# Kernel optimization log

Measured on AMD Instinct MI355X. Metric: run time of the kernel, lower is better.

Reference implementation:

```python
import jax, jax.numpy as jnp
import numpy as np

THRESH = 1e-6
EPS = 1e-8
LN_EPS = 1e-5


def _layer(h, M, W_in, b_in, W_out, b_out, W_self, b_self, gamma, beta):
    # Normalize incoming flows per destination column: A[j,i] = M[j,i]/sum_k M[k,i]
    A = M / (jnp.sum(M, axis=0, keepdims=True) + EPS)
    mask = A > THRESH
    W = jnp.where(mask, A, 0.0)                      # thresholded edge weights [N,N]
    T = h @ W_in + b_in                              # transformed features [N,out]
    weighted_sum = jnp.einsum('ji,jd->id', W, T)     # sum over origins j per dest i
    weight_sum = jnp.sum(W, axis=0)                  # [N]
    has_edge = jnp.any(mask, axis=0)                 # dest i has >=1 incoming edge
    agg = jnp.where(has_edge[:, None],
                    weighted_sum / (weight_sum[:, None] + EPS),
                    T)
    agg = agg @ W_out + b_out                        # dropout is identity in eval
    out = agg + (h @ W_self + b_self)                # residual (dims differ -> self_transform)
    mu = jnp.mean(out, axis=-1, keepdims=True)
    var = jnp.mean(jnp.square(out - mu), axis=-1, keepdims=True)
    out = (out - mu) * jax.lax.rsqrt(var + LN_EPS) * gamma + beta
    return out


def setup_inputs() -> dict:
    key = jax.random.key(0)
    ks = jax.random.split(key, 16)
    N, D_IN, D_H, D_OUT = 8192, 256, 512, 256
    s = 0.05
    return {
        'node_features': jax.random.normal(ks[0], (N, D_IN), jnp.float32),
        'mobility_matrix': jax.random.uniform(ks[1], (N, N), jnp.float32),
        # layer 1: in -> hidden
        'W_in1': jax.random.normal(ks[2], (D_IN, D_H)) * s,
        'b_in1': jnp.zeros((D_H,)),
        'W_out1': jax.random.normal(ks[3], (D_H, D_H)) * s,
        'b_out1': jnp.zeros((D_H,)),
        'W_self1': jax.random.normal(ks[4], (D_IN, D_H)) * s,
        'b_self1': jnp.zeros((D_H,)),
        'g1': jnp.ones((D_H,)),
        'be1': jnp.zeros((D_H,)),
        # layer 2: hidden -> out
        'W_in2': jax.random.normal(ks[5], (D_H, D_OUT)) * s,
        'b_in2': jnp.zeros((D_OUT,)),
        'W_out2': jax.random.normal(ks[6], (D_OUT, D_OUT)) * s,
        'b_out2': jnp.zeros((D_OUT,)),
        'W_self2': jax.random.normal(ks[7], (D_H, D_OUT)) * s,
        'b_self2': jnp.zeros((D_OUT,)),
        'g2': jnp.ones((D_OUT,)),
        'be2': jnp.zeros((D_OUT,)),
    }


def reference(node_features, mobility_matrix,
              W_in1, b_in1, W_out1, b_out1, W_self1, b_self1, g1, be1,
              W_in2, b_in2, W_out2, b_out2, W_self2, b_self2, g2, be2):
    h = _layer(node_features, mobility_matrix,
               W_in1, b_in1, W_out1, b_out1, W_self1, b_self1, g1, be1)
    h = jax.nn.relu(h)  # inter-layer activation
    h = _layer(h, mobility_matrix,
               W_in2, b_in2, W_out2, b_out2, W_self2, b_self2, g2, be2)
    h = jax.nn.relu(h)  # final activation
    return h
```

## Files before the change

### kernel.cpp

```cpp
#include <hip/hip_runtime.h>
#include <stdint.h>

typedef short bf16x8 __attribute__((ext_vector_type(8)));
typedef short s16x4 __attribute__((ext_vector_type(4)));
typedef float f32x4 __attribute__((ext_vector_type(4)));
typedef unsigned int u32;
typedef unsigned char u8;

#define EPS_A 1e-8f
#define THR_A 1e-6f
#define NN 8192

static __device__ __forceinline__ short f2bf(float f) {
  u32 u = __float_as_uint(f);
  u = u + 0x7FFFu + ((u >> 16) & 1u);
  return (short)(u >> 16);
}
static __device__ __forceinline__ float bf2f(short s) {
  return __uint_as_float(((u32)(unsigned short)s) << 16);
}
static __device__ __forceinline__ u8 f2fp8(float v) {
  return (u8)(__builtin_amdgcn_cvt_pk_fp8_f32(v, v, 0, false) & 0xff);
}
static __device__ __forceinline__ void gld16(const void* g, void* l) {
  __builtin_amdgcn_global_load_lds(
      (const __attribute__((address_space(1))) u32*)g,
      (__attribute__((address_space(3))) u32*)l, 16, 0, 0);
}

__global__ __launch_bounds__(256) void k_prep_all(
    const float* __restrict__ Mob, const float* __restrict__ nf,
    const float* __restrict__ W_in1, const float* __restrict__ W_out1,
    const float* __restrict__ W_self1, const float* __restrict__ W_in2,
    const float* __restrict__ W_out2, const float* __restrict__ W_self2,
    const float* __restrict__ b_in1, const float* __restrict__ b_out1,
    const float* __restrict__ b_self1, const float* __restrict__ b_out2,
    const float* __restrict__ b_self2,
    u8* __restrict__ Mt8, float* __restrict__ colsum, u32* __restrict__ colmax,
    u8* __restrict__ nft8, short* __restrict__ A1cat, short* __restrict__ Win1b,
    short* __restrict__ Wout1t, short* __restrict__ Bcat1, short* __restrict__ Win2t,
    short* __restrict__ Bcat2, float* __restrict__ bias1c, float* __restrict__ bias2c)
{
  __shared__ __align__(16) u32 sbuf[256 * 17];
  int b = blockIdx.x;
  const int t = threadIdx.x;
  if (b < 4096) {
    const int i0 = (b & 31) * 256;
    const int j0 = (b >> 5) * 64;
    const int i = i0 + t;
    float s = 0.f, mx = 0.f;
    #pragma unroll 4
    for (int j4 = 0; j4 < 16; ++j4) {
      float v0 = Mob[(size_t)(j0 + j4 * 4 + 0) * NN + i];
      float v1 = Mob[(size_t)(j0 + j4 * 4 + 1) * NN + i];
      float v2 = Mob[(size_t)(j0 + j4 * 4 + 2) * NN + i];
      float v3 = Mob[(size_t)(j0 + j4 * 4 + 3) * NN + i];
      s += v0 + v1 + v2 + v3;
      mx = fmaxf(fmaxf(mx, fmaxf(v0, v1)), fmaxf(v2, v3));
      u32 pk = __builtin_amdgcn_cvt_pk_fp8_f32(v0, v1, 0, false);
      pk = __builtin_amdgcn_cvt_pk_fp8_f32(v2, v3, (int)pk, true);
      sbuf[t * 17 + j4] = pk;
    }
    atomicAdd(&colsum[i], s);
    atomicMax(&colmax[i], __float_as_uint(mx));
    __syncthreads();
    #pragma unroll
    for (int p = 0; p < 4; ++p) {
      const int r = p * 64 + (t >> 2);
      const int c = t & 3;
      const u32* src = &sbuf[r * 17 + c * 4];
      int4 w = make_int4(src[0], src[1], src[2], src[3]);
      *(int4*)&Mt8[(size_t)(i0 + r) * NN + j0 + c * 16] = w;
    }
    return;
  }
  b -= 4096;
  if (b < 512) {
    u8* tile = (u8*)sbuf;
    const int r0 = (b & 127) * 64, c0 = (b >> 7) * 64;
    #pragma unroll
    for (int p = 0; p < 16; ++p) {
      const int rr = p * 4 + (t >> 6), cc = t & 63;
      tile[rr * 68 + cc] = f2fp8(nf[(size_t)(r0 + rr) * 256 + c0 + cc]);
    }
    __syncthreads();
    #pragma unroll
    for (int q = 0; q < 16; ++q) {
      const int cc = q * 4 + (t >> 6), rr = t & 63;
      nft8[(size_t)(c0 + cc) * 8192 + r0 + rr] = tile[rr * 68 + cc];
    }
    return;
  }
  b -= 512;
  if (b < 2048) {
    const int idx = b * 256 + t;
    const float4 v = ((const float4*)nf)[idx];
    const int i = idx >> 6;
    const int c = (idx & 63) * 4;
    s16x4 o;
    o.x = f2bf(v.x); o.y = f2bf(v.y); o.z = f2bf(v.z); o.w = f2bf(v.w);
    *(s16x4*)&A1cat[(size_t)i * 512 + 256 + c] = o;
    return;
  }
  b -= 2048;
  if (b < 128) {
    const int idx = b * 256 + t;
    const float4 v = ((const float4*)W_in1)[idx];
    s16x4 o;
    o.x = f2bf(v.x); o.y = f2bf(v.y); o.z = f2bf(v.z); o.w = f2bf(v.w);
    *(s16x4*)&Win1b[idx * 4] = o;
    return;
  }
  b -= 128;
  if (b < 1024) {
    const int idx = b * 256 + t;
    const int r = idx >> 9, c = idx & 511;
    Wout1t[(size_t)c * 512 + r] = f2bf(W_out1[idx]);
    return;
  }
  b -= 1024;
  if (b < 512) {
    const int idx = b * 256 + t;
    const int r = idx >> 9, c = idx & 511;
    Bcat1[(size_t)c * 512 + 256 + r] = f2bf(W_self1[idx]);
    return;
  }
  b -= 512;
  if (b < 512) {
    const int idx = b * 256 + t;
    const int r = idx >> 8, c = idx & 255;
    Win2t[(size_t)c * 512 + r] = f2bf(W_in2[idx]);
    return;
  }
  b -= 512;
  if (b < 256) {
    const int idx = b * 256 + t;
    const int r = idx >> 8, c = idx & 255;
    Bcat2[(size_t)c * 768 + r] = f2bf(W_out2[idx]);
    return;
  }
  b -= 256;
  if (b < 512) {
    const int idx = b * 256 + t;
    const int r = idx >> 8, c = idx & 255;
    Bcat2[(size_t)c * 768 + 256 + r] = f2bf(W_self2[idx]);
    return;
  }
  b -= 512;
  if (b < 2) {
    const int n = b * 256 + t;
    float a = b_out1[n] + b_self1[n];
    for (int p = 0; p < 512; ++p) a += b_in1[p] * W_out1[(size_t)p * 512 + n];
    bias1c[n] = a;
    return;
  }
  bias2c[t] = b_out2[t] + b_self2[t];
}

__global__ __launch_bounds__(256) void k_gemm_raw_n(
    const short* __restrict__ A, const short* __restrict__ B, int K, int ldA, int ldB,
    short* __restrict__ C, int ldC)
{
  constexpr int LDP = 40;
  __shared__ __align__(16) short As[64 * LDP];
  __shared__ __align__(16) short Bs[64 * LDP];
  const int t = threadIdx.x;
  const int m0 = blockIdx.y * 64, n0 = blockIdx.x * 64;
  const int wid = t >> 6, l = t & 63;
  const int wr = wid >> 1, wc = wid & 1;
  const int lr = l & 15, lk = l >> 4;
  f32x4 acc[2][2] = {};
  const int sr = t >> 2;
  const int sc = (t & 3) * 8;
  const short* gA0 = A + (size_t)(m0 + sr) * ldA + sc;
  const short* gB0 = B + (size_t)(n0 + sr) * ldB + sc;
  for (int k0 = 0; k0 < K; k0 += 32) {
    const int4 a0 = *(const int4*)(gA0 + k0);
    const int4 b0 = *(const int4*)(gB0 + k0);
    __syncthreads();
    *(int4*)&As[sr * LDP + sc] = a0;
    *(int4*)&Bs[sr * LDP + sc] = b0;
    __syncthreads();
    bf16x8 av[2], bv[2];
    #pragma unroll
    for (int mi = 0; mi < 2; ++mi)
      av[mi] = *(const bf16x8*)&As[(wr * 32 + mi * 16 + lr) * LDP + lk * 8];
    #pragma unroll
    for (int ni = 0; ni < 2; ++ni)
      bv[ni] = *(const bf16x8*)&Bs[(wc * 32 + ni * 16 + lr) * LDP + lk * 8];
    #pragma unroll
    for (int mi = 0; mi < 2; ++mi)
      #pragma unroll
      for (int ni = 0; ni < 2; ++ni)
        acc[mi][ni] = __builtin_amdgcn_mfma_f32_16x16x32_bf16(av[mi], bv[ni], acc[mi][ni], 0, 0, 0);
  }
  #pragma unroll
  for (int mi = 0; mi < 2; ++mi)
    #pragma unroll
    for (int r = 0; r < 4; ++r) {
      const int m = m0 + wr * 32 + mi * 16 + lk * 4 + r;
      #pragma unroll
      for (int ni = 0; ni < 2; ++ni) {
        const int n = n0 + wc * 32 + ni * 16 + lr;
        C[(size_t)m * ldC + n] = f2bf(acc[mi][ni][r]);
      }
    }
}

template <int BN, int EPI>
__global__ __launch_bounds__(256) void k_g64(
    const short* __restrict__ A, const short* __restrict__ B, int K, int ldA, int ldB,
    void* __restrict__ Cout, int ldC, const float* __restrict__ bias0,
    u8* __restrict__ C8)
{
  constexpr int ROWS = 64 + BN;
  constexpr int CH = ROWS / 32;
  constexpr int NI = BN / 32;
  __shared__ __align__(16) short S[ROWS * 64];
  const int t = threadIdx.x;

  const int gx = gridDim.x;
  int flat = blockIdx.y * gx + blockIdx.x;
  const int cpx = (gx * gridDim.y) >> 3;
  flat = (flat & 7) * cpx + (flat >> 3);
  const int bx = flat % gx, by = flat / gx;
  const int m0 = by * 64, n0 = bx * BN;

  const int wid = t >> 6, l = t & 63;
  const int wr = wid >> 1, wc = wid & 1;
  const int lr = l & 15, lk = l >> 4;

  f32x4 acc[2][NI] = {};

  const int lrow = l >> 3, lcol = l & 7;
  const int wbase = wid * (ROWS / 4);
  short* dbase = S + wbase * 64;
  const short* gsrc[CH];
  #pragma unroll
  for (int c = 0; c < CH; ++c) {
    const int ar = wbase + c * 8 + lrow;
    const int scol = (lcol ^ (ar & 7)) * 8;
    gsrc[c] = (ar < 64) ? A + (size_t)(m0 + ar) * ldA + scol
                        : B + (size_t)(n0 + ar - 64) * ldB + scol;
  }

  const int niters = K >> 6;
  int kk = flat % niters;
  for (int it = 0; it < niters; ++it) {
    const int koff = kk << 6;
    kk = (kk + 1 == niters) ? 0 : kk + 1;
    __syncthreads();
    #pragma unroll
    for (int c = 0; c < CH; ++c)
      gld16(gsrc[c] + koff, dbase + c * 512);
    __syncthreads();

    __builtin_amdgcn_s_setprio(1);
    #pragma unroll
    for (int ks = 0; ks < 2; ++ks) {
      bf16x8 av[2], bv[NI];
      #pragma unroll
      for (int mi = 0; mi < 2; ++mi) {
        const int row = wr * 32 + mi * 16 + lr;
        av[mi] = *(const bf16x8*)&S[row * 64 + ((ks * 4 + lk) ^ (row & 7)) * 8];
      }
      #pragma unroll
      for (int ni = 0; ni < NI; ++ni) {
        const int row = 64 + wc * (BN / 2) + ni * 16 + lr;
        bv[ni] = *(const bf16x8*)&S[row * 64 + ((ks * 4 + lk) ^ (row & 7)) * 8];
      }
      #pragma unroll
      for (int mi = 0; mi < 2; ++mi)
        #pragma unroll
        for (int ni = 0; ni < NI; ++ni)
          acc[mi][ni] = __builtin_amdgcn_mfma_f32_16x16x32_bf16(av[mi], bv[ni], acc[mi][ni], 0, 0, 0);
    }
    __builtin_amdgcn_s_setprio(0);
  }

  #pragma unroll
  for (int mi = 0; mi < 2; ++mi) {
    #pragma unroll
    for (int r = 0; r < 4; ++r) {
      const int m = m0 + wr * 32 + mi * 16 + lk * 4 + r;
      float bm = 0.f;
      if (EPI == 0 || EPI == 4) bm = bias0[m];
      #pragma unroll
      for (int ni = 0; ni < NI; ++ni) {
        const int n = n0 + wc * (BN / 2) + ni * 16 + lr;
        float v = acc[mi][ni][r];
        if (EPI == 0 || EPI == 4) {
          v += bm;
          ((short*)Cout)[(size_t)m * ldC + n] = f2bf(v);
          if (EPI == 4) C8[(size_t)m * ldC + n] = f2fp8(v);
        } else {
          ((float*)Cout)[(size_t)m * ldC + n] = v + bias0[n];
        }
      }
    }
  }
}

__global__ __launch_bounds__(256) void k_sk128_f8(
    const u8* __restrict__ A, const u8* __restrict__ B, int K, int ldA, int ldB,
    short* __restrict__ P, int ldC, size_t pstride)
{
  __shared__ __align__(16) u8 As[128 * 64];
  __shared__ __align__(16) u8 Bs[128 * 64];
  const int t = threadIdx.x;

  const int sk = blockIdx.z;
  A += (size_t)sk * K;
  B += (size_t)sk * K;

  const int gx = gridDim.x;
  int flat = blockIdx.y * gx + blockIdx.x;
  const int cpx = (gx * gridDim.y) >> 3;
  flat = (flat & 7) * cpx + (flat >> 3);
  const int bx = flat % gx, by = flat / gx;
  const int m0 = by * 128, n0 = bx * 128;

  const int wid = t >> 6, l = t & 63;
  const int wr = wid >> 1, wc = wid & 1;
  const int lr = l & 15, lk = l >> 4;

  f32x4 acc[4][4] = {};

  const int side = wid >> 1;
  const int hrow = (wid & 1) * 64;
  const u8* Xp = side ? B : A;
  const int ldX = side ? ldB : ldA;
  const int x0 = side ? n0 : m0;
  u8* dbase = (side ? Bs : As) + hrow * 64;
  const u8* gsrc[4];
  #pragma unroll
  for (int c = 0; c < 4; ++c) {
    const int row = hrow + c * 16 + (l >> 2);
    const int ql = (l & 3) ^ (row & 3);
    gsrc[c] = Xp + (size_t)(x0 + row) * ldX + ql * 16;
  }

  const int niters = K >> 6;
  int kk = (flat + sk * 3) & (niters - 1);
  for (int it = 0; it < niters; ++it) {
    const int koff = kk << 6;
    kk = (kk + 1) & (niters - 1);
    __syncthreads();
    gld16(gsrc[0] + koff, dbase);
    gld16(gsrc[1] + koff, dbase + 1024);
    gld16(gsrc[2] + koff, dbase + 2048);
    gld16(gsrc[3] + koff, dbase + 3072);
    __syncthreads();

    __builtin_amdgcn_s_setprio(1);
    #pragma unroll
    for (int ks = 0; ks < 2; ++ks) {
      const int q = ks * 2 + (lk >> 1);
      const int inner = (lk & 1) * 8;
      long av[4], bv[4];
      #pragma unroll
      for (int mi = 0; mi < 4; ++mi) {
        const int row = wr * 64 + mi * 16 + lr;
        av[mi] = *(const long*)&As[row * 64 + ((q ^ (row & 3)) << 4) + inner];
      }
      #pragma unroll
      for (int ni = 0; ni < 4; ++ni) {
        const int row = wc * 64 + ni * 16 + lr;
        bv[ni] = *(const long*)&Bs[row * 64 + ((q ^ (row & 3)) << 4) + inner];
      }
      #pragma unroll
      for (int mi = 0; mi < 4; ++mi)
        #pragma unroll
        for (int ni = 0; ni < 4; ++ni)
          acc[mi][ni] = __builtin_amdgcn_mfma_f32_16x16x32_fp8_fp8(av[mi], bv[ni], acc[mi][ni], 0, 0, 0);
    }
    __builtin_amdgcn_s_setprio(0);
  }

  short* outp = P + pstride * sk;
  #pragma unroll
  for (int mi = 0; mi < 4; ++mi) {
    #pragma unroll
    for (int r = 0; r < 4; ++r) {
      const int m = m0 + wr * 64 + mi * 16 + lk * 4 + r;
      #pragma unroll
      for (int ni = 0; ni < 4; ++ni) {
        const int n = n0 + wc * 64 + ni * 16 + lr;
        outp[(size_t)m * ldC + n] = f2bf(acc[mi][ni][r]);
      }
    }
  }
}

__global__ __launch_bounds__(256) void k_sk_reduce_sub(
    const short* __restrict__ P, int N, size_t pstride, int S,
    const float* __restrict__ colsum, const u32* __restrict__ colmax,
    const short* __restrict__ hraw, int ldh,
    short* __restrict__ out, int ldo)
{
  const int idx = blockIdx.x * 256 + threadIdx.x;
  const int nq = N >> 2;
  const int m = idx / nq;
  const int c4 = (idx - m * nq) * 4;
  const size_t base = (size_t)m * N + c4;
  float a0 = 0.f, a1 = 0.f, a2 = 0.f, a3 = 0.f;
  for (int s = 0; s < S; ++s) {
    s16x4 v = *(const s16x4*)&P[pstride * s + base];
    a0 += bf2f(v.x); a1 += bf2f(v.y); a2 += bf2f(v.z); a3 += bf2f(v.w);
  }
  const float cs = colsum[m];
  const float rc = 1.f / (cs + EPS_A);
  const float rcw = rc / (cs * rc + EPS_A);
  const bool he = __uint_as_float(colmax[m]) * rc > THR_A;
  s16x4 o;
  if (he) {
    o.x = f2bf(a0 * rcw); o.y = f2bf(a1 * rcw);
    o.z = f2bf(a2 * rcw); o.w = f2bf(a3 * rcw);
  } else {
    o = *(const s16x4*)&hraw[(size_t)m * ldh + c4];
  }
  *(s16x4*)&out[(size_t)m * ldo + c4] = o;
}

__global__ __launch_bounds__(256) void k_sk_reduce(
    const short* __restrict__ P, int N, size_t pstride, int S,
    const float* __restrict__ colsum, const u32* __restrict__ colmax,
    const short* __restrict__ Tfall, short* __restrict__ out, int ldo)
{
  const int idx = blockIdx.x * 256 + threadIdx.x;
  const int nq = N >> 2;
  const int m = idx / nq;
  const int c4 = (idx - m * nq) * 4;
  const size_t base = (size_t)m * N + c4;
  float a0 = 0.f, a1 = 0.f, a2 = 0.f, a3 = 0.f;
  for (int s = 0; s < S; ++s) {
    s16x4 v = *(const s16x4*)&P[pstride * s + base];
    a0 += bf2f(v.x); a1 += bf2f(v.y); a2 += bf2f(v.z); a3 += bf2f(v.w);
  }
  const float cs = colsum[m];
  const float rc = 1.f / (cs + EPS_A);
  const float rcw = rc / (cs * rc + EPS_A);
  const bool he = __uint_as_float(colmax[m]) * rc > THR_A;
  a0 *= rcw; a1 *= rcw; a2 *= rcw; a3 *= rcw;
  if (__ballot(!he)) {
    if (!he) {
      a0 = bf2f(Tfall[(size_t)(c4 + 0) * NN + m]);
      a1 = bf2f(Tfall[(size_t)(c4 + 1) * NN + m]);
      a2 = bf2f(Tfall[(size_t)(c4 + 2) * NN + m]);
      a3 = bf2f(Tfall[(size_t)(c4 + 3) * NN + m]);
    }
  }
  s16x4 o;
  o.x = f2bf(a0); o.y = f2bf(a1); o.z = f2bf(a2); o.w = f2bf(a3);
  *(s16x4*)&out[(size_t)m * ldo + c4] = o;
}

template <int MODE>
__device__ __forceinline__ void ln_relu_body(
    const float* __restrict__ X, int W,
    const float* __restrict__ g, const float* __restrict__ be,
    void* __restrict__ out, int ldo)
{
  const int row = blockIdx.x;
  const int t = threadIdx.x;
  const float* x = X + (size_t)row * W;
  float v0 = x[t], v1 = 0.f;
  float s = v0, ss = v0 * v0;
  if (W == 512) { v1 = x[t + 256]; s += v1; ss += v1 * v1; }
  #pragma unroll
  for (int off = 32; off; off >>= 1) {
    s += __shfl_down(s, off);
    ss += __shfl_down(ss, off);
  }
  __shared__ float red[8];
  const int wid = t >> 6;
  if ((t & 63) == 0) { red[wid] = s; red[4 + wid] = ss; }
  __syncthreads();
  s = red[0] + red[1] + red[2] + red[3];
  ss = red[4] + red[5] + red[6] + red[7];
  const float mu = s / W;
  const float var = ss / W - mu * mu;
  const float sc = rsqrtf(var + 1e-5f);
  float y = fmaxf((v0 - mu) * sc * g[t] + be[t], 0.f);
  if (MODE == 0) ((short*)out)[(size_t)row * ldo + t] = f2bf(y);
  else           ((float*)out)[(size_t)row * ldo + t] = y;
  if (W == 512) {
    float y1 = fmaxf((v1 - mu) * sc * g[t + 256] + be[t + 256], 0.f);
    if (MODE == 0) ((short*)out)[(size_t)row * ldo + t + 256] = f2bf(y1);
    else           ((float*)out)[(size_t)row * ldo + t + 256] = y1;
  }
}

__global__ __launch_bounds__(256) void k_ln_relu_bf16(
    const float* __restrict__ X, int W, const float* __restrict__ g,
    const float* __restrict__ be, short* __restrict__ out, int ldo) {
  ln_relu_body<0>(X, W, g, be, out, ldo);
}
__global__ __launch_bounds__(256) void k_ln_relu_f32(
    const float* __restrict__ X, int W, const float* __restrict__ g,
    const float* __restrict__ be, float* __restrict__ out, int ldo) {
  ln_relu_body<1>(X, W, g, be, out, ldo);
}

extern "C" void kernel_launch(void* const* d_in, const int* in_sizes, int n_in,
                              void* d_out, int out_size, void* d_ws, size_t ws_size,
                              hipStream_t stream) {
  const float* nf      = (const float*)d_in[0];
  const float* Mob     = (const float*)d_in[1];
  const float* W_in1   = (const float*)d_in[2];
  const float* b_in1   = (const float*)d_in[3];
  const float* W_out1  = (const float*)d_in[4];
  const float* b_out1  = (const float*)d_in[5];
  const float* W_self1 = (const float*)d_in[6];
  const float* b_self1 = (const float*)d_in[7];
  const float* g1      = (const float*)d_in[8];
  const float* be1     = (const float*)d_in[9];
  const float* W_in2   = (const float*)d_in[10];
  const float* b_in2   = (const float*)d_in[11];
  const float* W_out2  = (const float*)d_in[12];
  const float* b_out2  = (const float*)d_in[13];
  const float* W_self2 = (const float*)d_in[14];
  const float* b_self2 = (const float*)d_in[15];
  const float* g2      = (const float*)d_in[16];
  const float* be2     = (const float*)d_in[17];

  char* ws = (char*)d_ws;
  float* colsum = (float*)(ws);
  u32*   colmax = (u32*)(ws + 32768);
  u8*    Mt8    = (u8*)(ws + 131072);
  u8*    nft8   = (u8*)(ws + 67239936);
  u8*    T2t8   = (u8*)(ws + 69337088);
  short* A1cat  = (short*)(ws + 71434240);
  float* C2f    = (float*)(ws + 79822848);
  short* Acat2  = (short*)(ws + 96600064);
  short* T2t    = (short*)(ws + 109182976);
  short* Bcat1  = (short*)(ws + 113377280);
  short* Bcat2  = (short*)(ws + 113901568);
  short* Win2t  = (short*)(ws + 114294784);
  short* Wout1t = (short*)(ws + 114556928);
  short* Win1b  = (short*)(ws + 115081216);
  float* bias1c = (float*)(ws + 115343360);
  float* bias2c = (float*)(ws + 115345408);
  short* P1     = (short*)(ws + 117440512);
  short* P2     = (short*)(ws + 150994944);

  hipMemsetAsync(ws, 0, 65536, stream);

  k_prep_all<<<9603, 256, 0, stream>>>(Mob, nf, W_in1, W_out1, W_self1, W_in2,
                                       W_out2, W_self2, b_in1, b_out1, b_self1,
                                       b_out2, b_self2, Mt8, colsum, colmax, nft8,
                                       A1cat, Win1b, Wout1t, Bcat1, Win2t, Bcat2,
                                       bias1c, bias2c);
  k_gemm_raw_n<<<dim3(4, 8), 256, 0, stream>>>(Wout1t, Win1b, 512, 512, 512,
                                               Bcat1, 512);

  k_sk128_f8<<<dim3(2, 64, 8), 256, 0, stream>>>(Mt8, nft8, 1024, NN, NN,
                                                 P1, 256, (size_t)8192 * 256);
  k_sk_reduce_sub<<<2048, 256, 0, stream>>>(P1, 256, (size_t)8192 * 256, 8,
                                            colsum, colmax, A1cat + 256, 512,
                                            A1cat, 512);
  k_g64<128, 2><<<dim3(4, 128), 256, 0, stream>>>(A1cat, Bcat1, 512, 512, 512,
                                                  C2f, 512, bias1c, nullptr);
  k_ln_relu_bf16<<<8192, 256, 0, stream>>>(C2f, 512, g1, be1, Acat2 + 256, 768);

  k_g64<64, 4><<<dim3(128, 4), 256, 0, stream>>>(Win2t, Acat2 + 256, 512, 512, 768,
                                                 T2t, NN, b_in2, T2t8);
  k_sk128_f8<<<dim3(2, 64, 8), 256, 0, stream>>>(Mt8, T2t8, 1024, NN, NN,
                                                 P2, 256, (size_t)8192 * 256);
  k_sk_reduce<<<2048, 256, 0, stream>>>(P2, 256, (size_t)8192 * 256, 8,
                                        colsum, colmax, T2t, Acat2, 768);
  k_g64<64, 2><<<dim3(4, 128), 256, 0, stream>>>(Acat2, Bcat2, 768, 768, 768,
                                                 C2f, 256, bias2c, nullptr);
  k_ln_relu_f32<<<8192, 256, 0, stream>>>(C2f, 256, g2, be2, (float*)d_out, 256);
}
```

Baseline: 278.9 us.

## Double-buffer LDS tiles in fp8 split-K GEMM to overlap loads with MFMA

Splits the shared-memory staging into two 16 KB buffers and prefetches the next K-tile through direct global-to-LDS loads while the current tile is consumed by MFMAs. Partial vmcnt waits and raw s_barrier calls replace the two full __syncthreads per iteration. This is meant to hide global load latency behind compute, at the cost of twice the LDS per block, which may reduce occupancy. It also depends on the hand-written vmcnt counting being correct.

```diff
diff --git a/kernel.cpp b/kernel.cpp
--- a/kernel.cpp
+++ b/kernel.cpp
@@ -305,8 +305,7 @@
     const u8* __restrict__ A, const u8* __restrict__ B, int K, int ldA, int ldB,
     short* __restrict__ P, int ldC, size_t pstride)
 {
-  __shared__ __align__(16) u8 As[128 * 64];
-  __shared__ __align__(16) u8 Bs[128 * 64];
+  __shared__ __align__(16) u8 S[2][16384];
   const int t = threadIdx.x;
 
   const int sk = blockIdx.z;
@@ -331,7 +330,9 @@
   const u8* Xp = side ? B : A;
   const int ldX = side ? ldB : ldA;
   const int x0 = side ? n0 : m0;
-  u8* dbase = (side ? Bs : As) + hrow * 64;
+  const int doff = side * 8192 + hrow * 64;
+  u8* d0 = &S[0][doff];
+  u8* d1 = &S[1][doff];
   const u8* gsrc[4];
   #pragma unroll
   for (int c = 0; c < 4; ++c) {
@@ -342,16 +343,34 @@
 
   const int niters = K >> 6;
   int kk = (flat + sk * 3) & (niters - 1);
-  for (int it = 0; it < niters; ++it) {
+  {
     const int koff = kk << 6;
     kk = (kk + 1) & (niters - 1);
-    __syncthreads();
-    gld16(gsrc[0] + koff, dbase);
-    gld16(gsrc[1] + koff, dbase + 1024);
-    gld16(gsrc[2] + koff, dbase + 2048);
-    gld16(gsrc[3] + koff, dbase + 3072);
-    __syncthreads();
-
+    gld16(gsrc[0] + koff, d0);
+    gld16(gsrc[1] + koff, d0 + 1024);
+    gld16(gsrc[2] + koff, d0 + 2048);
+    gld16(gsrc[3] + koff, d0 + 3072);
+  }
+
+  int buf = 0;
+  for (int it = 0; it < niters; ++it) {
+    if (it + 1 < niters) {
+      const int koff = kk << 6;
+      kk = (kk + 1) & (niters - 1);
+      u8* nb = buf ? d0 : d1;
+      gld16(gsrc[0] + koff, nb);
+      gld16(gsrc[1] + koff, nb + 1024);
+      gld16(gsrc[2] + koff, nb + 2048);
+      gld16(gsrc[3] + koff, nb + 3072);
+      asm volatile("s_waitcnt vmcnt(4)" ::: "memory");
+    } else {
+      asm volatile("s_waitcnt vmcnt(0)" ::: "memory");
+    }
+    __builtin_amdgcn_sched_barrier(0);
+    __builtin_amdgcn_s_barrier();
+
+    const u8* Ab = &S[buf][0];
+    const u8* Bb = &S[buf][8192];
     __builtin_amdgcn_s_setprio(1);
     #pragma unroll
     for (int ks = 0; ks < 2; ++ks) {
@@ -361,12 +380,12 @@
       #pragma unroll
       for (int mi = 0; mi < 4; ++mi) {
         const int row = wr * 64 + mi * 16 + lr;
-        av[mi] = *(const long*)&As[row * 64 + ((q ^ (row & 3)) << 4) + inner];
+        av[mi] = *(const long*)&Ab[row * 64 + ((q ^ (row & 3)) << 4) + inner];
       }
       #pragma unroll
       for (int ni = 0; ni < 4; ++ni) {
         const int row = wc * 64 + ni * 16 + lr;
-        bv[ni] = *(const long*)&Bs[row * 64 + ((q ^ (row & 3)) << 4) + inner];
+        bv[ni] = *(const long*)&Bb[row * 64 + ((q ^ (row & 3)) << 4) + inner];
       }
       #pragma unroll
       for (int mi = 0; mi < 4; ++mi)
@@ -375,6 +394,8 @@
           acc[mi][ni] = __builtin_amdgcn_mfma_f32_16x16x32_fp8_fp8(av[mi], bv[ni], acc[mi][ni], 0, 0, 0);
     }
     __builtin_amdgcn_s_setprio(0);
+    __builtin_amdgcn_s_barrier();
+    buf ^= 1;
   }
 
   short* outp = P + pstride * sk;
```

After: 266.1 us. 1.05x faster.
